# Optimization experiments

Measured on AMD Instinct MI355X. Metric: run time of the kernel, lower is better.

## Reference

```python
import jax, jax.numpy as jnp
import numpy as np

EPS = 1e-6
INPUTS = 1836
LABELS = 159
NUM_VALS = 2
HIDDEN = 1024
BATCH = 8192
ITERS = 20          # cfg.inference.iterations
INF_LR = 1.0        # cfg.inference.learning_rate (sqrt decay)
ENT_COEF = 1.0      # cfg.entropy_coef


def setup_inputs() -> dict:
    key = jax.random.key(0)
    ks = jax.random.split(key, 8)
    f32 = jnp.float32
    xs = jax.random.normal(ks[0], (BATCH, INPUTS), f32)
    # feature MLP: 1836 -> 150 -> 150 -> 159 (weights ~ N(0, 2/fan_in), bias 0)
    Wf1 = jax.random.normal(ks[1], (150, INPUTS), f32) * np.sqrt(2.0 / INPUTS).astype(np.float32)
    bf1 = jnp.zeros((150,), f32)
    Wf2 = jax.random.normal(ks[2], (150, 150), f32) * np.sqrt(2.0 / 150).astype(np.float32)
    bf2 = jnp.zeros((150,), f32)
    Wf3 = jax.random.normal(ks[3], (LABELS, 150), f32) * np.sqrt(2.0 / 150).astype(np.float32)
    bf3 = jnp.zeros((LABELS,), f32)
    # global energy net: Linear(159->1024, no bias), Softplus, Linear(1024->1, no bias)
    Wg1 = jax.random.normal(ks[4], (HIDDEN, LABELS), f32) * (1.0 / np.sqrt(LABELS)).astype(np.float32)
    Wg2 = jax.random.normal(ks[5], (1, HIDDEN), f32) * (1.0 / np.sqrt(HIDDEN)).astype(np.float32)
    return dict(xs=xs, Wf1=Wf1, bf1=bf1, Wf2=Wf2, bf2=bf2, Wf3=Wf3, bf3=bf3, Wg1=Wg1, Wg2=Wg2)


def _init_pred(batch_size):
    # _random_probabilities: sorted-uniform stick-breaking, shared across the batch
    x = jax.random.uniform(jax.random.key(1), (LABELS, NUM_VALS + 1), jnp.float32)
    x = x.at[:, 0].set(0.0).at[:, -1].set(1.0)
    x = jnp.sort(x, axis=1)
    p = x[:, 1:] - x[:, :-1]                       # (LABELS, NUM_VALS), rows sum to 1
    return jnp.broadcast_to(p[None], (batch_size, LABELS, NUM_VALS))


def reference(xs, Wf1, bf1, Wf2, bf2, Wf3, bf3, Wg1, Wg2):
    # feature energy network -> potentials (B, LABELS, 2), channel 0 is zero
    h = jax.nn.relu(xs @ Wf1.T + bf1)
    h = jax.nn.relu(h @ Wf2.T + bf2)
    logits = h @ Wf3.T + bf3                        # (B, LABELS)
    potentials = jnp.stack([jnp.zeros_like(logits), logits], axis=-1)  # (B, LABELS, 2)

    def energy_sum(pred):
        # sum over batch of: <pred, potentials> + Wg2 softplus(Wg1 pred[:,:,1]) - c*H-term
        ge = jnp.sum(pred * potentials)
        le = jnp.sum(jax.nn.softplus(pred[:, :, 1] @ Wg1.T) @ Wg2.T)
        ent = jnp.sum(pred * jnp.log(pred + EPS))
        return ge + le - ENT_COEF * ent

    egrad = jax.grad(energy_sum)

    def step(pred, it):
        g = egrad(pred)                             # (B, LABELS, NUM_VALS)
        lr = INF_LR / jnp.sqrt(it.astype(jnp.float32))
        lg = lr * g
        m = jnp.max(lg, axis=-1, keepdims=True)     # stabilized multiplicative update
        p = pred * jnp.exp(lg - m)
        p = p / (jnp.sum(p, axis=-1, keepdims=True) + EPS)
        return p, None

    pred0 = _init_pred(xs.shape[0])
    pred, _ = jax.lax.scan(step, pred0, jnp.arange(1, ITERS))
    return pred
```

## Files before the change

kernel.cpp:

```cpp
#include <hip/hip_runtime.h>
#include <hip/hip_bf16.h>
#include <math.h>

#define EPSF 1e-6f
#define NLBL 159
#define NLP  160
#define HID  1024
#define BATCH 8192
#define MROWS 32
#define PBS  168
#define SBS  1044
#define K1   1836
#define K1P  1856
#define NF   150
#define NFP  160

typedef __attribute__((ext_vector_type(8))) short short8v;
typedef __attribute__((ext_vector_type(4))) float f32x4;

__device__ inline ushort f2bf(float f) {
  __hip_bfloat16 h = __float2bfloat16(f);
  return *reinterpret_cast<ushort*>(&h);
}
__device__ inline float bf2f(ushort u) {
  unsigned v = ((unsigned)u) << 16;
  return __uint_as_float(v);
}
__device__ inline float rcpf(float x) { return __builtin_amdgcn_rcpf(x); }
__device__ inline float sigmoidf(float x) { return rcpf(1.0f + __expf(-x)); }

__device__ __forceinline__ void dma16(const void* g, void* l) {
  __builtin_amdgcn_global_load_lds(
      (const __attribute__((address_space(1))) unsigned int*)g,
      (__attribute__((address_space(3))) unsigned int*)l, 16, 0, 0);
}

__device__ inline unsigned rotl32(unsigned x, int d){ return (x<<d)|(x>>(32-d)); }

__device__ inline void threefry2x32(unsigned k0, unsigned k1,
                                    unsigned x0, unsigned x1,
                                    unsigned* o0, unsigned* o1) {
  unsigned ks0=k0, ks1=k1, ks2=k0^k1^0x1BD11BDAu;
  x0 += ks0; x1 += ks1;
#define TF_R(r) { x0 += x1; x1 = rotl32(x1,(r)); x1 ^= x0; }
  TF_R(13) TF_R(15) TF_R(26) TF_R(6)  x0 += ks1; x1 += ks2 + 1u;
  TF_R(17) TF_R(29) TF_R(16) TF_R(24) x0 += ks2; x1 += ks0 + 2u;
  TF_R(13) TF_R(15) TF_R(26) TF_R(6)  x0 += ks0; x1 += ks1 + 3u;
  TF_R(17) TF_R(29) TF_R(16) TF_R(24) x0 += ks1; x1 += ks2 + 4u;
  TF_R(13) TF_R(15) TF_R(26) TF_R(6)  x0 += ks2; x1 += ks0 + 5u;
#undef TF_R
  *o0 = x0; *o1 = x1;
}

template<int RELU>
__global__ __launch_bounds__(256) void gemm_xwt(const float* __restrict__ A,
                                                const float* __restrict__ W,
                                                const float* __restrict__ bias,
                                                float* __restrict__ C,
                                                int M, int N, int K) {
  __shared__ float As[32][68];
  __shared__ float Ws[32][68];
  const int tid = threadIdx.x;
  const int m0 = blockIdx.x * 64;
  const int n0 = blockIdx.y * 64;
  const int tn = tid & 15;
  const int tm = tid >> 4;
  float acc[4][4];
#pragma unroll
  for (int i=0;i<4;++i)
#pragma unroll
    for (int j=0;j<4;++j) acc[i][j]=0.f;

  for (int k0 = 0; k0 < K; k0 += 32) {
    __syncthreads();
#pragma unroll
    for (int s2 = 0; s2 < 8; ++s2) {
      int f = tid + s2*256;
      int kk = f & 31, mm = f >> 5;
      int k = k0 + kk;
      float av = 0.f, wvv = 0.f;
      if (k < K) {
        av = A[(size_t)(m0+mm)*K + k];
        int n = n0 + mm;
        if (n < N) wvv = W[(size_t)n*K + k];
      }
      As[kk][mm] = av;
      Ws[kk][mm] = wvv;
    }
    __syncthreads();
    for (int kk=0; kk<32; ++kk) {
      float4 a4 = *(const float4*)&As[kk][tm*4];
      float4 b4 = *(const float4*)&Ws[kk][tn*4];
      float ai[4] = {a4.x,a4.y,a4.z,a4.w};
      float bj[4] = {b4.x,b4.y,b4.z,b4.w};
#pragma unroll
      for (int i=0;i<4;++i)
#pragma unroll
        for (int j=0;j<4;++j) acc[i][j] = fmaf(ai[i], bj[j], acc[i][j]);
    }
  }
#pragma unroll
  for (int i=0;i<4;++i)
#pragma unroll
    for (int j=0;j<4;++j) {
      int m = m0 + tm*4 + i;
      int n = n0 + tn*4 + j;
      if (n < N) {
        float v = acc[i][j] + bias[n];
        if (RELU) v = fmaxf(v, 0.f);
        C[(size_t)m*N + n] = v;
      }
    }
}

__global__ void prep_weights(const float* __restrict__ Wg1,
                             ushort* __restrict__ Wg1b,
                             ushort* __restrict__ Wg1Tb) {
  int idx = blockIdx.x*256 + threadIdx.x;
  if (idx >= HID*NLP) return;
  int h = idx / NLP, l = idx % NLP;
  float v = (l < NLBL) ? Wg1[h*NLBL + l] : 0.f;
  ushort b = f2bf(v);
  Wg1b[h*NLP + l]  = b;
  Wg1Tb[l*HID + h] = b;
}

__global__ void prep_wf1(const float* __restrict__ Wf1,
                         ushort* __restrict__ Wh, ushort* __restrict__ Wl) {
  int idx = blockIdx.x*256 + threadIdx.x;
  if (idx >= NFP*K1P) return;
  int n = idx / K1P, k = idx % K1P;
  float v = (n < NF && k < K1) ? Wf1[n*K1 + k] : 0.f;
  ushort h = f2bf(v);
  Wh[idx] = h;
  Wl[idx] = f2bf(v - bf2f(h));
}

__global__ __launch_bounds__(256) void gemm1_split(
    const float* __restrict__ xs, const ushort* __restrict__ Wh,
    const ushort* __restrict__ Wl, const float* __restrict__ bias,
    float* __restrict__ h1) {
  __shared__ float Asf[32*36];
  const int tid = threadIdx.x;
  const int wv = tid >> 6, lane = tid & 63;
  const int c = lane & 15, g = lane >> 4;
  const int row0 = blockIdx.x * 32;
  const int ntc = (wv < 2) ? 3 : 2;
  const int ntv[3] = {wv, wv + 4, wv + 8};

  f32x4 acc[3][2];
#pragma unroll
  for (int t = 0; t < 3; ++t)
#pragma unroll
    for (int rt = 0; rt < 2; ++rt) acc[t][rt] = (f32x4){0.f,0.f,0.f,0.f};

  const int srow = tid >> 3;
  const int skof = (tid & 7) * 4;

  for (int ks = 0; ks < K1P/32; ++ks) {
    const int k0 = ks * 32;
    const int ksrc = k0 + skof;
    const float4 av = *(const float4*)&xs[(size_t)(row0 + srow)*K1 + ((ksrc < K1) ? ksrc : 0)];
    __syncthreads();
    *(float4*)&Asf[srow*36 + skof] = av;
    __syncthreads();
    short8v ah[2], al[2];
#pragma unroll
    for (int rt = 0; rt < 2; ++rt) {
      const float* ap = &Asf[(rt*16 + c)*36 + g*8];
      float4 x0 = *(const float4*)ap;
      float4 x1 = *(const float4*)(ap + 4);
      float xv[8] = {x0.x,x0.y,x0.z,x0.w,x1.x,x1.y,x1.z,x1.w};
#pragma unroll
      for (int j = 0; j < 8; ++j) {
        ushort hh = f2bf(xv[j]);
        ah[rt][j] = (short)hh;
        al[rt][j] = (short)f2bf(xv[j] - bf2f(hh));
      }
    }
#pragma unroll
    for (int t = 0; t < 3; ++t) {
      if (t >= ntc) break;
      const int n = ntv[t]*16 + c;
      const size_t wo = (size_t)n*K1P + k0 + g*8;
      short8v wh = *(const short8v*)&Wh[wo];
      short8v wl = *(const short8v*)&Wl[wo];
#pragma unroll
      for (int rt = 0; rt < 2; ++rt) {
        acc[t][rt] = __builtin_amdgcn_mfma_f32_16x16x32_bf16(ah[rt], wh, acc[t][rt], 0, 0, 0);
        acc[t][rt] = __builtin_amdgcn_mfma_f32_16x16x32_bf16(ah[rt], wl, acc[t][rt], 0, 0, 0);
        acc[t][rt] = __builtin_amdgcn_mfma_f32_16x16x32_bf16(al[rt], wh, acc[t][rt], 0, 0, 0);
      }
    }
  }
#pragma unroll
  for (int t = 0; t < 3; ++t) {
    if (t >= ntc) break;
    const int n = ntv[t]*16 + c;
    if (n < NF) {
      const float bv = bias[n];
#pragma unroll
      for (int rt = 0; rt < 2; ++rt)
#pragma unroll
        for (int r = 0; r < 4; ++r) {
          int m = row0 + rt*16 + g*4 + r;
          h1[(size_t)m*NF + n] = fmaxf(acc[t][rt][r] + bv, 0.f);
        }
    }
  }
}

__global__ __launch_bounds__(512, 2) void spen_iter_mfma(
    const float* __restrict__ logits,
    const ushort* __restrict__ Wg1b,
    const ushort* __restrict__ Wg1Tb,
    const float* __restrict__ Wg2,
    float* __restrict__ out) {
  __shared__ __align__(16) ushort ring[2][20480];
  __shared__ ushort p1b[MROWS*PBS];
  __shared__ ushort s_b[MROWS*SBS];
  __shared__ float  u_s[NLBL];

  const int tid  = threadIdx.x;
  const int wv   = tid >> 6;
  const int lane = tid & 63;
  const int col  = lane & 15;
  const int kg   = lane >> 4;
  const int row0 = blockIdx.x * MROWS;

  if (tid < NLBL) {
    unsigned i = 3u*(unsigned)tid + 1u;
    unsigned x0, x1; bool use1;
    if (i < 239u) { x0 = i; x1 = (i == 238u) ? 0u : (239u + i); use1 = false; }
    else          { x0 = i - 239u; x1 = i; use1 = true; }
    unsigned o0, o1;
    threefry2x32(0u, 1u, x0, x1, &o0, &o1);
    unsigned bits = use1 ? o1 : o0;
    u_s[tid] = __uint_as_float((bits >> 9) | 0x3f800000u) - 1.0f;
  }
  __syncthreads();
  for (int idx = tid; idx < MROWS*NLP; idx += 512) {
    int m = idx / NLP, l = idx % NLP;
    float p1 = (l < NLBL) ? (1.0f - u_s[l]) : 0.f;
    p1b[m*PBS + l] = f2bf(p1);
  }

  const bool has2 = (wv < 2);
  const int l0 = wv*16 + col;
  const int l1 = 128 + wv*16 + col;
  const bool v1 = has2 && (l1 < NLBL);

  float q0[8], q1[8];
  {
    float u0v = u_s[l0];
    float qi0 = __logf((1.0f - u0v) * rcpf(u0v));
    float qi1 = 0.f;
    if (v1) { float u1v = u_s[l1]; qi1 = __logf((1.0f - u1v) * rcpf(u1v)); }
#pragma unroll
    for (int i = 0; i < 8; ++i) { q0[i] = qi0; q1[i] = qi1; }
  }

  float wg2own[8];
#pragma unroll
  for (int c = 0; c < 8; ++c) wg2own[c] = Wg2[(c*8 + wv)*16 + col];

  float lg0[8], lg1[8];
#pragma unroll
  for (int rh = 0; rh < 2; ++rh)
#pragma unroll
    for (int r = 0; r < 4; ++r) {
      int m = row0 + rh*16 + kg*4 + r;
      lg0[rh*4+r] = logits[(size_t)m*NLBL + l0];
      lg1[rh*4+r] = v1 ? logits[(size_t)m*NLBL + l1] : 0.f;
    }

  const char* wg1b_bytes = (const char*)Wg1b;
  const ushort* sp0 = &s_b[col*SBS + kg*8];
  const ushort* sp1 = &s_b[(16 + col)*SBS + kg*8];
  const ushort* wt0 = &Wg1Tb[(size_t)l0*HID + kg*8];
  const ushort* wt1 = &Wg1Tb[(size_t)l1*HID + kg*8];

  {
    const char* g = wg1b_bytes + wv*5120 + lane*16;
#pragma unroll
    for (int i = 0; i < 5; ++i)
      dma16(g + i*1024, (char*)&ring[0][wv*2560] + i*1024);
  }

  for (int it = 1; it <= 19; ++it) {
    const float lr = rsqrtf((float)it);
    __syncthreads();
    short8v afr0[5], afr1[5];
#pragma unroll
    for (int kk = 0; kk < 5; ++kk) {
      afr0[kk] = *(const short8v*)&p1b[col*PBS + kk*32 + kg*8];
      afr1[kk] = *(const short8v*)&p1b[(16 + col)*PBS + kk*32 + kg*8];
    }
#pragma unroll
    for (int c = 0; c < 8; ++c) {
      if (c < 7) {
        const char* g = wg1b_bytes + (size_t)(c+1)*40960 + wv*5120 + lane*16;
        char* l = (char*)&ring[(c+1)&1][wv*2560];
#pragma unroll
        for (int i = 0; i < 5; ++i)
          dma16(g + i*1024, l + i*1024);
        asm volatile("s_waitcnt vmcnt(5)" ::: "memory");
      } else {
        asm volatile("s_waitcnt vmcnt(0)" ::: "memory");
      }
      __builtin_amdgcn_sched_barrier(0);
      const ushort* wtile = &ring[c&1][wv*2560];
      f32x4 a0 = (f32x4){0.f,0.f,0.f,0.f};
      f32x4 a1 = (f32x4){0.f,0.f,0.f,0.f};
#pragma unroll
      for (int kk = 0; kk < 5; ++kk) {
        short8v bf = *(const short8v*)&wtile[col*160 + kk*32 + kg*8];
        a0 = __builtin_amdgcn_mfma_f32_16x16x32_bf16(afr0[kk], bf, a0, 0, 0, 0);
        a1 = __builtin_amdgcn_mfma_f32_16x16x32_bf16(afr1[kk], bf, a1, 0, 0, 0);
      }
      const int h = c*128 + wv*16 + col;
      const float g2 = wg2own[c];
#pragma unroll
      for (int r = 0; r < 4; ++r) {
        s_b[(kg*4 + r)*SBS + h]      = f2bf(g2 * sigmoidf(a0[r]));
        s_b[(16 + kg*4 + r)*SBS + h] = f2bf(g2 * sigmoidf(a1[r]));
      }
    }
    short8v wrA[2][4], wrB[2][4];
#pragma unroll
    for (int j = 0; j < 4; ++j) wrA[0][j] = *(const short8v*)(wt0 + j*32);
    if (has2) {
#pragma unroll
      for (int j = 0; j < 4; ++j) wrB[0][j] = *(const short8v*)(wt1 + j*32);
    }
    __syncthreads();
    if (it < 19) {
      const char* g = wg1b_bytes + wv*5120 + lane*16;
#pragma unroll
      for (int i = 0; i < 5; ++i)
        dma16(g + i*1024, (char*)&ring[0][wv*2560] + i*1024);
    }
    f32x4 bA0 = (f32x4){0.f,0.f,0.f,0.f};
    f32x4 bA1 = (f32x4){0.f,0.f,0.f,0.f};
    f32x4 bB0 = (f32x4){0.f,0.f,0.f,0.f};
    f32x4 bB1 = (f32x4){0.f,0.f,0.f,0.f};
    if (has2) {
#pragma unroll
      for (int b = 0; b < 8; ++b) {
        const int cur = b & 1;
        if (b < 7) {
#pragma unroll
          for (int j = 0; j < 4; ++j) {
            wrA[cur^1][j] = *(const short8v*)(wt0 + ((b+1)*4 + j)*32);
            wrB[cur^1][j] = *(const short8v*)(wt1 + ((b+1)*4 + j)*32);
          }
        }
#pragma unroll
        for (int j = 0; j < 4; ++j) {
          const int kk = b*4 + j;
          short8v a0 = *(const short8v*)(sp0 + kk*32);
          short8v a1 = *(const short8v*)(sp1 + kk*32);
          bA0 = __builtin_amdgcn_mfma_f32_16x16x32_bf16(a0, wrA[cur][j], bA0, 0, 0, 0);
          bA1 = __builtin_amdgcn_mfma_f32_16x16x32_bf16(a1, wrA[cur][j], bA1, 0, 0, 0);
          bB0 = __builtin_amdgcn_mfma_f32_16x16x32_bf16(a0, wrB[cur][j], bB0, 0, 0, 0);
          bB1 = __builtin_amdgcn_mfma_f32_16x16x32_bf16(a1, wrB[cur][j], bB1, 0, 0, 0);
        }
      }
    } else {
#pragma unroll
      for (int b = 0; b < 8; ++b) {
        const int cur = b & 1;
        if (b < 7) {
#pragma unroll
          for (int j = 0; j < 4; ++j)
            wrA[cur^1][j] = *(const short8v*)(wt0 + ((b+1)*4 + j)*32);
        }
#pragma unroll
        for (int j = 0; j < 4; ++j) {
          const int kk = b*4 + j;
          short8v a0 = *(const short8v*)(sp0 + kk*32);
          short8v a1 = *(const short8v*)(sp1 + kk*32);
          bA0 = __builtin_amdgcn_mfma_f32_16x16x32_bf16(a0, wrA[cur][j], bA0, 0, 0, 0);
          bA1 = __builtin_amdgcn_mfma_f32_16x16x32_bf16(a1, wrA[cur][j], bA1, 0, 0, 0);
        }
      }
    }
#define UPDATE_ONE(QARR, IDX, LGV, BK, LL, MM)                               \
    {                                                                        \
      float q = QARR[IDX];                                                   \
      float p1v = sigmoidf(q);                                               \
      float p0v = 1.0f - p1v;                                                \
      float rp1 = rcpf(p1v + EPSF);                                          \
      float rp0 = rcpf(p0v + EPSF);                                          \
      float dlt = (LGV) + (BK) - __logf((p1v + EPSF)*rp0) - p1v*rp1 + p0v*rp0;\
      q += lr*dlt;                                                           \
      QARR[IDX] = q;                                                         \
      p1b[(MM)*PBS + (LL)] = f2bf(sigmoidf(q));                              \
    }
#pragma unroll
    for (int r = 0; r < 4; ++r) {
      const int m0r = kg*4 + r;
      UPDATE_ONE(q0, r, lg0[r], bA0[r], l0, m0r)
      const int m1r = 16 + kg*4 + r;
      UPDATE_ONE(q0, 4 + r, lg0[4 + r], bA1[r], l0, m1r)
    }
    if (v1) {
#pragma unroll
      for (int r = 0; r < 4; ++r) {
        const int m0r = kg*4 + r;
        UPDATE_ONE(q1, r, lg1[r], bB0[r], l1, m0r)
        const int m1r = 16 + kg*4 + r;
        UPDATE_ONE(q1, 4 + r, lg1[4 + r], bB1[r], l1, m1r)
      }
    }
#undef UPDATE_ONE
  }

#pragma unroll
  for (int rh = 0; rh < 2; ++rh)
#pragma unroll
    for (int r = 0; r < 4; ++r) {
      const int row = row0 + rh*16 + kg*4 + r;
      float p1v = sigmoidf(q0[rh*4 + r]);
      size_t o = ((size_t)row*NLBL + l0)*2;
      out[o]   = 1.0f - p1v;
      out[o+1] = p1v;
      if (v1) {
        float p1w = sigmoidf(q1[rh*4 + r]);
        size_t o2 = ((size_t)row*NLBL + l1)*2;
        out[o2]   = 1.0f - p1w;
        out[o2+1] = p1w;
      }
    }
}

extern "C" void kernel_launch(void* const* d_in, const int* in_sizes, int n_in,
                              void* d_out, int out_size, void* d_ws, size_t ws_size,
                              hipStream_t stream) {
  const float* xs  = (const float*)d_in[0];
  const float* Wf1 = (const float*)d_in[1];
  const float* bf1 = (const float*)d_in[2];
  const float* Wf2 = (const float*)d_in[3];
  const float* bf2 = (const float*)d_in[4];
  const float* Wf3 = (const float*)d_in[5];
  const float* bf3 = (const float*)d_in[6];
  const float* Wg1 = (const float*)d_in[7];
  const float* Wg2 = (const float*)d_in[8];
  float* out = (float*)d_out;

  float* h1     = (float*)d_ws;
  float* h2     = h1 + (size_t)BATCH*NF;
  float* logits = h2 + (size_t)BATCH*NF;
  ushort* Wg1b  = (ushort*)(logits + (size_t)BATCH*NLBL);
  ushort* Wg1Tb = Wg1b + (size_t)HID*NLP;
  ushort* Wf1h  = Wg1Tb + (size_t)NLP*HID;
  ushort* Wf1l  = Wf1h + (size_t)NFP*K1P;

  prep_wf1<<<(NFP*K1P + 255)/256, 256, 0, stream>>>(Wf1, Wf1h, Wf1l);
  prep_weights<<<(HID*NLP + 255)/256, 256, 0, stream>>>(Wg1, Wg1b, Wg1Tb);

  gemm1_split<<<BATCH/32, 256, 0, stream>>>(xs, Wf1h, Wf1l, bf1, h1);
  gemm_xwt<1><<<dim3(BATCH/64, 3), 256, 0, stream>>>(h1, Wf2, bf2, h2, BATCH, NF, NF);
  gemm_xwt<0><<<dim3(BATCH/64, 3), 256, 0, stream>>>(h2, Wf3, bf3, logits, BATCH, NLBL, NF);

  spen_iter_mfma<<<BATCH/MROWS, 512, 0, stream>>>(logits, Wg1b, Wg1Tb, Wg2, out);
}
```

Before: 511.7 us.

## Fuse three feature MLP layers into one kernel using split-bf16 MFMA

Replaces the separate first-layer GEMM and the two scalar fp32 GEMMs for layers 2 and 3 with one fused kernel. Hidden activations stay in shared memory as hi/lo bf16 pairs, and layers 2 and 3 run on MFMA with the three-product split-bf16 scheme. This removes two kernel launches and the global round trips for h1 and h2, and moves the small GEMMs onto matrix cores. It adds a weight-prep kernel and more shared memory per block, which may lower occupancy, and the split-bf16 products are slightly less exact than the fp32 FMAs they replace.

```diff
diff --git a/kernel.cpp b/kernel.cpp
--- a/kernel.cpp
+++ b/kernel.cpp
@@ -52,67 +52,6 @@
   *o0 = x0; *o1 = x1;
 }
 
-template<int RELU>
-__global__ __launch_bounds__(256) void gemm_xwt(const float* __restrict__ A,
-                                                const float* __restrict__ W,
-                                                const float* __restrict__ bias,
-                                                float* __restrict__ C,
-                                                int M, int N, int K) {
-  __shared__ float As[32][68];
-  __shared__ float Ws[32][68];
-  const int tid = threadIdx.x;
-  const int m0 = blockIdx.x * 64;
-  const int n0 = blockIdx.y * 64;
-  const int tn = tid & 15;
-  const int tm = tid >> 4;
-  float acc[4][4];
-#pragma unroll
-  for (int i=0;i<4;++i)
-#pragma unroll
-    for (int j=0;j<4;++j) acc[i][j]=0.f;
-
-  for (int k0 = 0; k0 < K; k0 += 32) {
-    __syncthreads();
-#pragma unroll
-    for (int s2 = 0; s2 < 8; ++s2) {
-      int f = tid + s2*256;
-      int kk = f & 31, mm = f >> 5;
-      int k = k0 + kk;
-      float av = 0.f, wvv = 0.f;
-      if (k < K) {
-        av = A[(size_t)(m0+mm)*K + k];
-        int n = n0 + mm;
-        if (n < N) wvv = W[(size_t)n*K + k];
-      }
-      As[kk][mm] = av;
-      Ws[kk][mm] = wvv;
-    }
-    __syncthreads();
-    for (int kk=0; kk<32; ++kk) {
-      float4 a4 = *(const float4*)&As[kk][tm*4];
-      float4 b4 = *(const float4*)&Ws[kk][tn*4];
-      float ai[4] = {a4.x,a4.y,a4.z,a4.w};
-      float bj[4] = {b4.x,b4.y,b4.z,b4.w};
-#pragma unroll
-      for (int i=0;i<4;++i)
-#pragma unroll
-        for (int j=0;j<4;++j) acc[i][j] = fmaf(ai[i], bj[j], acc[i][j]);
-    }
-  }
-#pragma unroll
-  for (int i=0;i<4;++i)
-#pragma unroll
-    for (int j=0;j<4;++j) {
-      int m = m0 + tm*4 + i;
-      int n = n0 + tn*4 + j;
-      if (n < N) {
-        float v = acc[i][j] + bias[n];
-        if (RELU) v = fmaxf(v, 0.f);
-        C[(size_t)m*N + n] = v;
-      }
-    }
-}
-
 __global__ void prep_weights(const float* __restrict__ Wg1,
                              ushort* __restrict__ Wg1b,
                              ushort* __restrict__ Wg1Tb) {
@@ -136,11 +75,29 @@
   Wl[idx] = f2bf(v - bf2f(h));
 }
 
-__global__ __launch_bounds__(256) void gemm1_split(
-    const float* __restrict__ xs, const ushort* __restrict__ Wh,
-    const ushort* __restrict__ Wl, const float* __restrict__ bias,
-    float* __restrict__ h1) {
+__global__ void prep_w23(const float* __restrict__ Wf2, const float* __restrict__ Wf3,
+                         ushort* __restrict__ W2h, ushort* __restrict__ W2l,
+                         ushort* __restrict__ W3h, ushort* __restrict__ W3l) {
+  int idx = blockIdx.x*256 + threadIdx.x;
+  if (idx >= NFP*NFP) return;
+  int n = idx / NFP, k = idx % NFP;
+  float v2 = (n < NF && k < NF) ? Wf2[n*NF + k] : 0.f;
+  ushort h2 = f2bf(v2);
+  W2h[idx] = h2; W2l[idx] = f2bf(v2 - bf2f(h2));
+  float v3 = (n < NLBL && k < NF) ? Wf3[n*NF + k] : 0.f;
+  ushort h3 = f2bf(v3);
+  W3h[idx] = h3; W3l[idx] = f2bf(v3 - bf2f(h3));
+}
+
+__global__ __launch_bounds__(256) void mlp_fused(
+    const float* __restrict__ xs,
+    const ushort* __restrict__ W1h, const ushort* __restrict__ W1l, const float* __restrict__ b1,
+    const ushort* __restrict__ W2h, const ushort* __restrict__ W2l, const float* __restrict__ b2,
+    const ushort* __restrict__ W3h, const ushort* __restrict__ W3l, const float* __restrict__ b3,
+    float* __restrict__ logits) {
   __shared__ float Asf[32*36];
+  __shared__ ushort h1h[32*168], h1l[32*168];
+  __shared__ ushort h2h[32*168], h2l[32*168];
   const int tid = threadIdx.x;
   const int wv = tid >> 6, lane = tid & 63;
   const int c = lane & 15, g = lane >> 4;
@@ -183,8 +140,8 @@
       if (t >= ntc) break;
       const int n = ntv[t]*16 + c;
       const size_t wo = (size_t)n*K1P + k0 + g*8;
-      short8v wh = *(const short8v*)&Wh[wo];
-      short8v wl = *(const short8v*)&Wl[wo];
+      short8v wh = *(const short8v*)&W1h[wo];
+      short8v wl = *(const short8v*)&W1l[wo];
 #pragma unroll
       for (int rt = 0; rt < 2; ++rt) {
         acc[t][rt] = __builtin_amdgcn_mfma_f32_16x16x32_bf16(ah[rt], wh, acc[t][rt], 0, 0, 0);
@@ -193,18 +150,111 @@
       }
     }
   }
+  __syncthreads();
 #pragma unroll
   for (int t = 0; t < 3; ++t) {
     if (t >= ntc) break;
     const int n = ntv[t]*16 + c;
-    if (n < NF) {
-      const float bv = bias[n];
+    const float bv = (n < NF) ? b1[n] : 0.f;
+#pragma unroll
+    for (int rt = 0; rt < 2; ++rt)
+#pragma unroll
+      for (int r = 0; r < 4; ++r) {
+        const int m = rt*16 + g*4 + r;
+        float v = (n < NF) ? fmaxf(acc[t][rt][r] + bv, 0.f) : 0.f;
+        ushort hi = f2bf(v);
+        h1h[m*168 + n] = hi;
+        h1l[m*168 + n] = f2bf(v - bf2f(hi));
+      }
+  }
+  __syncthreads();
+
+  f32x4 a2[3][2];
+#pragma unroll
+  for (int t = 0; t < 3; ++t)
+#pragma unroll
+    for (int rt = 0; rt < 2; ++rt) a2[t][rt] = (f32x4){0.f,0.f,0.f,0.f};
+#pragma unroll
+  for (int kk = 0; kk < 5; ++kk) {
+    short8v ah[2], al[2];
+#pragma unroll
+    for (int rt = 0; rt < 2; ++rt) {
+      ah[rt] = *(const short8v*)&h1h[(rt*16 + c)*168 + kk*32 + g*8];
+      al[rt] = *(const short8v*)&h1l[(rt*16 + c)*168 + kk*32 + g*8];
+    }
+#pragma unroll
+    for (int t = 0; t < 3; ++t) {
+      if (t >= ntc) break;
+      const int n = ntv[t]*16 + c;
+      const size_t wo = (size_t)n*NFP + kk*32 + g*8;
+      short8v wh = *(const short8v*)&W2h[wo];
+      short8v wl = *(const short8v*)&W2l[wo];
+#pragma unroll
+      for (int rt = 0; rt < 2; ++rt) {
+        a2[t][rt] = __builtin_amdgcn_mfma_f32_16x16x32_bf16(ah[rt], wh, a2[t][rt], 0, 0, 0);
+        a2[t][rt] = __builtin_amdgcn_mfma_f32_16x16x32_bf16(ah[rt], wl, a2[t][rt], 0, 0, 0);
+        a2[t][rt] = __builtin_amdgcn_mfma_f32_16x16x32_bf16(al[rt], wh, a2[t][rt], 0, 0, 0);
+      }
+    }
+  }
+#pragma unroll
+  for (int t = 0; t < 3; ++t) {
+    if (t >= ntc) break;
+    const int n = ntv[t]*16 + c;
+    const float bv = (n < NF) ? b2[n] : 0.f;
+#pragma unroll
+    for (int rt = 0; rt < 2; ++rt)
+#pragma unroll
+      for (int r = 0; r < 4; ++r) {
+        const int m = rt*16 + g*4 + r;
+        float v = (n < NF) ? fmaxf(a2[t][rt][r] + bv, 0.f) : 0.f;
+        ushort hi = f2bf(v);
+        h2h[m*168 + n] = hi;
+        h2l[m*168 + n] = f2bf(v - bf2f(hi));
+      }
+  }
+  __syncthreads();
+
+  f32x4 a3[3][2];
+#pragma unroll
+  for (int t = 0; t < 3; ++t)
+#pragma unroll
+    for (int rt = 0; rt < 2; ++rt) a3[t][rt] = (f32x4){0.f,0.f,0.f,0.f};
+#pragma unroll
+  for (int kk = 0; kk < 5; ++kk) {
+    short8v ah[2], al[2];
+#pragma unroll
+    for (int rt = 0; rt < 2; ++rt) {
+      ah[rt] = *(const short8v*)&h2h[(rt*16 + c)*168 + kk*32 + g*8];
+      al[rt] = *(const short8v*)&h2l[(rt*16 + c)*168 + kk*32 + g*8];
+    }
+#pragma unroll
+    for (int t = 0; t < 3; ++t) {
+      if (t >= ntc) break;
+      const int n = ntv[t]*16 + c;
+      const size_t wo = (size_t)n*NFP + kk*32 + g*8;
+      short8v wh = *(const short8v*)&W3h[wo];
+      short8v wl = *(const short8v*)&W3l[wo];
+#pragma unroll
+      for (int rt = 0; rt < 2; ++rt) {
+        a3[t][rt] = __builtin_amdgcn_mfma_f32_16x16x32_bf16(ah[rt], wh, a3[t][rt], 0, 0, 0);
+        a3[t][rt] = __builtin_amdgcn_mfma_f32_16x16x32_bf16(ah[rt], wl, a3[t][rt], 0, 0, 0);
+        a3[t][rt] = __builtin_amdgcn_mfma_f32_16x16x32_bf16(al[rt], wh, a3[t][rt], 0, 0, 0);
+      }
+    }
+  }
+#pragma unroll
+  for (int t = 0; t < 3; ++t) {
+    if (t >= ntc) break;
+    const int n = ntv[t]*16 + c;
+    if (n < NLBL) {
+      const float bv = b3[n];
 #pragma unroll
       for (int rt = 0; rt < 2; ++rt)
 #pragma unroll
         for (int r = 0; r < 4; ++r) {
-          int m = row0 + rt*16 + g*4 + r;
-          h1[(size_t)m*NF + n] = fmaxf(acc[t][rt][r] + bv, 0.f);
+          const int m = row0 + rt*16 + g*4 + r;
+          logits[(size_t)m*NLBL + n] = a3[t][rt][r] + bv;
         }
     }
   }
@@ -448,20 +498,23 @@
   const float* Wg2 = (const float*)d_in[8];
   float* out = (float*)d_out;
 
-  float* h1     = (float*)d_ws;
-  float* h2     = h1 + (size_t)BATCH*NF;
-  float* logits = h2 + (size_t)BATCH*NF;
+  float* logits = (float*)d_ws;
   ushort* Wg1b  = (ushort*)(logits + (size_t)BATCH*NLBL);
   ushort* Wg1Tb = Wg1b + (size_t)HID*NLP;
   ushort* Wf1h  = Wg1Tb + (size_t)NLP*HID;
   ushort* Wf1l  = Wf1h + (size_t)NFP*K1P;
+  ushort* Wf2h  = Wf1l + (size_t)NFP*K1P;
+  ushort* Wf2l  = Wf2h + (size_t)NFP*NFP;
+  ushort* Wf3h  = Wf2l + (size_t)NFP*NFP;
+  ushort* Wf3l  = Wf3h + (size_t)NFP*NFP;
 
   prep_wf1<<<(NFP*K1P + 255)/256, 256, 0, stream>>>(Wf1, Wf1h, Wf1l);
+  prep_w23<<<(NFP*NFP + 255)/256, 256, 0, stream>>>(Wf2, Wf3, Wf2h, Wf2l, Wf3h, Wf3l);
   prep_weights<<<(HID*NLP + 255)/256, 256, 0, stream>>>(Wg1, Wg1b, Wg1Tb);
 
-  gemm1_split<<<BATCH/32, 256, 0, stream>>>(xs, Wf1h, Wf1l, bf1, h1);
-  gemm_xwt<1><<<dim3(BATCH/64, 3), 256, 0, stream>>>(h1, Wf2, bf2, h2, BATCH, NF, NF);
-  gemm_xwt<0><<<dim3(BATCH/64, 3), 256, 0, stream>>>(h2, Wf3, bf3, logits, BATCH, NLBL, NF);
+  mlp_fused<<<BATCH/32, 256, 0, stream>>>(xs, Wf1h, Wf1l, bf1,
+                                          Wf2h, Wf2l, bf2,
+                                          Wf3h, Wf3l, bf3, logits);
 
   spen_iter_mfma<<<BATCH/MROWS, 512, 0, stream>>>(logits, Wg1b, Wg1Tb, Wg2, out);
 }
```

New measurement: 486.0 us, median of 2. -5.0%, faster.
